# Performance work log

Measured on AMD Instinct MI355X. Metric: run time of the kernel, lower is better.

## Reference

```python
import jax, jax.numpy as jnp
import numpy as np

D_MODEL = 768


def setup_inputs() -> dict:
    key = jax.random.key(0)
    ks = jax.random.split(key, 16)
    B, S, D = 8, 2048, D_MODEL
    scale = 1.0 / np.sqrt(D)
    inp = {
        "Z_graph": jax.random.normal(ks[0], (B, S, D), dtype=jnp.float32),
        "Z_lstm": jax.random.normal(ks[1], (B, S, D), dtype=jnp.float32),
    }
    names = ["Wqg", "Wkl", "Wvl", "Wql", "Wkg", "Wvg", "Wf"]
    for i, n in enumerate(names):
        inp[n] = jax.random.uniform(ks[2 + i], (D, D), dtype=jnp.float32,
                                    minval=-scale, maxval=scale)
        inp["b" + n[1:]] = jax.random.uniform(ks[9 + i], (D,), dtype=jnp.float32,
                                              minval=-scale, maxval=scale)
    return inp


def reference(Z_graph, Z_lstm, Wqg, bqg, Wkl, bkl, Wvl, bvl,
              Wql, bql, Wkg, bkg, Wvg, bvg, Wf, bf):
    D = Z_graph.shape[-1]
    inv_sqrt_d = 1.0 / jnp.sqrt(jnp.asarray(D, dtype=Z_graph.dtype))

    def lin(x, W, b):
        # torch nn.Linear: x @ W.T + b
        return jnp.einsum("bsd,ed->bse", x, W) + b

    # graph -> lstm attention
    Qg = lin(Z_graph, Wqg, bqg)
    Kl = lin(Z_lstm, Wkl, bkl)
    Vl = lin(Z_lstm, Wvl, bvl)
    attn_g2l = jax.nn.softmax(
        jnp.einsum("bqd,bkd->bqk", Qg, Kl) * inv_sqrt_d, axis=-1)
    Z_g2l = jnp.einsum("bqk,bkd->bqd", attn_g2l, Vl)

    # lstm -> graph attention
    Ql = lin(Z_lstm, Wql, bql)
    Kg = lin(Z_graph, Wkg, bkg)
    Vg = lin(Z_graph, Wvg, bvg)
    attn_l2g = jax.nn.softmax(
        jnp.einsum("bqd,bkd->bqk", Ql, Kg) * inv_sqrt_d, axis=-1)
    Z_l2g = jnp.einsum("bqk,bkd->bqd", attn_l2g, Vg)

    Z_fused = Z_g2l + Z_l2g
    return lin(Z_fused, Wf, bf)
```

## Files before the change

kernel.cpp:

```cpp
#include <hip/hip_runtime.h>
#include <math.h>

#define TILE 128
#define BK   64
#define NT   256

typedef __attribute__((ext_vector_type(8))) short bf16x8;
typedef __attribute__((ext_vector_type(4))) float f32x4;

typedef const __attribute__((address_space(1))) void* gvp;
typedef __attribute__((address_space(3))) void* lvp;

__device__ __forceinline__ float bf2f(unsigned short u) {
  union { unsigned int i; float f; } v; v.i = ((unsigned int)u) << 16; return v.f;
}
__device__ __forceinline__ unsigned short f2bf(float f) {
  union { float ff; unsigned int i; } v; v.ff = f;
  return (unsigned short)((v.i + 0x7fffu + ((v.i >> 16) & 1u)) >> 16);
}

__device__ __forceinline__ int xcd_swz(int h, int nwg) {
  int q = nwg >> 3, r = nwg & 7;
  int xcd = h & 7, pos = h >> 3;
  return (xcd < r ? xcd * (q + 1) : r * (q + 1) + (xcd - r) * q) + pos;
}

struct GemmSrc { const unsigned short* A; int lda; const unsigned short* B; int ldb; int nk; };

__device__ __forceinline__ void stage_tile(const unsigned short* g, int ld, int r0, int k0,
                                           short* lds, int tid) {
#pragma unroll
  for (int i = 0; i < 4; ++i) {
    int cid = i * NT + tid;
    int row = cid >> 3, kc = cid & 7;
    int kcs = kc ^ (row & 7);
    const unsigned short* src = g + (size_t)(r0 + row) * ld + (k0 + kcs * 8);
    __builtin_amdgcn_global_load_lds((gvp)src, (lvp)(lds + cid * 8), 16, 0, 0);
  }
}

__device__ __forceinline__ void compute_tile(const short* As, const short* Bs,
                                             f32x4 acc[4][4], int lr, int lk, int wm, int wn) {
#pragma unroll
  for (int kk = 0; kk < 2; ++kk) {
    bf16x8 a[4], b[4];
#pragma unroll
    for (int i = 0; i < 4; ++i) {
      int ra = wm * 64 + i * 16 + lr;
      int rb = wn * 64 + i * 16 + lr;
      int ca = ((kk * 4 + lk) ^ (ra & 7)) * 8;
      int cb = ((kk * 4 + lk) ^ (rb & 7)) * 8;
      a[i] = *(const bf16x8*)(As + ra * BK + ca);
      b[i] = *(const bf16x8*)(Bs + rb * BK + cb);
    }
#pragma unroll
    for (int i = 0; i < 4; ++i)
#pragma unroll
      for (int j = 0; j < 4; ++j)
        acc[i][j] = __builtin_amdgcn_mfma_f32_16x16x32_bf16(a[i], b[j], acc[i][j], 0, 0, 0);
  }
}

template<int NS>
__device__ __forceinline__ void gemm_accum(const GemmSrc* s, f32x4 acc[4][4],
                                           short* As, short* Bs, int tid, int r0, int c0) {
  int lane = tid & 63, w = tid >> 6;
  int lr = lane & 15, lk = lane >> 4;
  int wm = w >> 1, wn = w & 1;
#pragma unroll
  for (int si = 0; si < NS; ++si) {
    int nk = s[si].nk;
    for (int kt = 0; kt < nk; ++kt) {
      __syncthreads();
      stage_tile(s[si].A, s[si].lda, r0, kt * BK, As, tid);
      stage_tile(s[si].B, s[si].ldb, c0, kt * BK, Bs, tid);
      __syncthreads();
      compute_tile(As, Bs, acc, lr, lk, wm, wn);
    }
  }
}

__device__ __forceinline__ void gemm_accum_pair(const unsigned short* A, int lda,
                                                const unsigned short* B, int ldb, int nk,
                                                f32x4 acc[4][4],
                                                short* A0, short* B0, short* A1, short* B1,
                                                int tid, int r0, int c0) {
  int lane = tid & 63, w = tid >> 6;
  int lr = lane & 15, lk = lane >> 4;
  int wm = w >> 1, wn = w & 1;
  for (int kt = 0; kt < nk / 2; ++kt) {
    __syncthreads();
    stage_tile(A, lda, r0, (2 * kt) * BK,     A0, tid);
    stage_tile(B, ldb, c0, (2 * kt) * BK,     B0, tid);
    stage_tile(A, lda, r0, (2 * kt + 1) * BK, A1, tid);
    stage_tile(B, ldb, c0, (2 * kt + 1) * BK, B1, tid);
    __syncthreads();
    compute_tile(A0, B0, acc, lr, lk, wm, wn);
    compute_tile(A1, B1, acc, lr, lk, wm, wn);
  }
}

template<bool OUT_BF16, bool BIAS_N, bool BIAS_M>
__device__ __forceinline__ void gemm_epilogue(f32x4 acc[4][4], void* C, int ldc,
                                              int r0, int c0, const float* bias,
                                              float alpha, int tid) {
  int lane = tid & 63, w = tid >> 6;
  int lr = lane & 15, lk = lane >> 4;
  int wm = w >> 1, wn = w & 1;
#pragma unroll
  for (int i = 0; i < 4; ++i) {
#pragma unroll
    for (int j = 0; j < 4; ++j) {
      int col = c0 + wn * 64 + j * 16 + lr;
      float bn = BIAS_N ? bias[col] : 0.f;
#pragma unroll
      for (int r = 0; r < 4; ++r) {
        int row = r0 + wm * 64 + i * 16 + lk * 4 + r;
        float v = acc[i][j][r] * alpha + bn;
        if (BIAS_M) v += bias[row];
        size_t idx = (size_t)row * ldc + col;
        if (OUT_BF16) ((unsigned short*)C)[idx] = f2bf(v);
        else          ((float*)C)[idx] = v;
      }
    }
  }
}

__device__ __forceinline__ void zero_acc(f32x4 acc[4][4]) {
  f32x4 z = { 0.f, 0.f, 0.f, 0.f };
#pragma unroll
  for (int i = 0; i < 4; ++i)
#pragma unroll
    for (int j = 0; j < 4; ++j) acc[i][j] = z;
}


struct ConvW { const float* src[7]; unsigned short* dst[7]; };

__global__ __launch_bounds__(NT) void k_convert_w(ConvW a) {
  int z = blockIdx.y;
  const float* s = a.src[z];
  unsigned short* d = a.dst[z];
  const int n = 768 * 768;
  int stride = gridDim.x * NT * 4;
  for (int i = ((int)blockIdx.x * NT + (int)threadIdx.x) * 4; i < n; i += stride) {
    float4 f = *(const float4*)(s + i);
    ushort4 o;
    o.x = f2bf(f.x); o.y = f2bf(f.y); o.z = f2bf(f.z); o.w = f2bf(f.w);
    *(ushort4*)(d + i) = o;
  }
}

__global__ __launch_bounds__(NT) void k_convert_z(const float* zg, const float* zl,
                                                  unsigned short* dg, unsigned short* dl,
                                                  float* lsum, int nL,
                                                  long long off, int n) {
  if (blockIdx.y == 0) {
    int fid = ((int)blockIdx.x * NT + (int)threadIdx.x) * 4;
    if (fid < nL) *(float4*)(lsum + fid) = make_float4(0.f, 0.f, 0.f, 0.f);
  }
  const float* s = (blockIdx.y ? zl : zg) + off;
  unsigned short* d = blockIdx.y ? dl : dg;
  int stride = gridDim.x * NT * 4;
  for (int i = ((int)blockIdx.x * NT + (int)threadIdx.x) * 4; i < n; i += stride) {
    float4 f = *(const float4*)(s + i);
    ushort4 o;
    o.x = f2bf(f.x); o.y = f2bf(f.y); o.z = f2bf(f.z); o.w = f2bf(f.w);
    *(ushort4*)(d + i) = o;
  }
}

struct ProjAllArgs {
  const unsigned short* A[6];
  const unsigned short* B[6];
  const float* bias[6];
  unsigned short* dst[6];
  int SG;
};

__global__ __launch_bounds__(512) void k_projall(ProjAllArgs p) {
  __shared__ __align__(16) short lds[4][TILE * BK];
  int nwg = (int)gridDim.x;
  int l = xcd_swz((int)blockIdx.x, nwg);
  int tpz = nwg / 6;
  int z = l / tpz, t = l % tpz;
  int grp = (int)threadIdx.x >> 8;
  int gt  = (int)threadIdx.x & 255;
  bool vt = (z >= 4);
  int r0, c0;
  if (!vt) { r0 = (t / 3) * TILE; c0 = ((t % 3) * 2 + grp) * TILE; }
  else     { r0 = ((t % 3) * 2 + grp) * TILE; c0 = (t / 3) * TILE; }
  f32x4 acc[4][4]; zero_acc(acc);
  GemmSrc s = { p.A[z], 768, p.B[z], 768, 768 / BK };
  gemm_accum<1>(&s, acc, lds[grp * 2], lds[grp * 2 + 1], gt, r0, c0);
  if (!vt)
    gemm_epilogue<true, true, false>(acc, p.dst[z], 768, r0, c0, p.bias[z], 1.f, gt);
  else
    gemm_epilogue<true, false, true>(acc, p.dst[z], p.SG, r0, c0, p.bias[z], 1.f, gt);
}

__global__ __launch_bounds__(512) void k_scores(const unsigned short* Qg, const unsigned short* Kl,
                                                const unsigned short* Ql, const unsigned short* Kg,
                                                unsigned short* S, float* lsum,
                                                float alpha, int G) {
  __shared__ __align__(16) short lds[4][TILE * BK];
  int nwg = (int)(gridDim.x * gridDim.y * gridDim.z);
  int h = (int)blockIdx.x + (int)gridDim.x * ((int)blockIdx.y + (int)gridDim.y * (int)blockIdx.z);
  int l = xcd_swz(h, nwg);
  int xp = l & 7, y = (l >> 3) & 15, z = l >> 7;
  int grp = (int)threadIdx.x >> 8;
  int gt  = (int)threadIdx.x & 255;
  int x = xp * 2 + grp;
  int dir = (z >= G) ? 1 : 0, gi = z - dir * G;
  const unsigned short* Q = (dir ? Ql : Qg) + (size_t)gi * 2048 * 768;
  const unsigned short* K = (dir ? Kg : Kl) + (size_t)gi * 2048 * 768;
  unsigned short* C = S + (size_t)z * 2048 * 2048;
  float* lrow = lsum + (size_t)z * 2048;
  int r0 = y * TILE, c0 = x * TILE;
  int lane = gt & 63, w = gt >> 6;
  int lr = lane & 15, lk = lane >> 4, wm = w >> 1, wn = w & 1;
  f32x4 acc[4][4]; zero_acc(acc);
  GemmSrc s = { Q, 768, K, 768, 768 / BK };
  gemm_accum<1>(&s, acc, lds[grp * 2], lds[grp * 2 + 1], gt, r0, c0);
  __syncthreads();
  short* Es = lds[grp * 2];
#pragma unroll
  for (int i = 0; i < 4; ++i) {
    float rs[4] = { 0.f, 0.f, 0.f, 0.f };
#pragma unroll
    for (int j = 0; j < 4; ++j) {
      int lcol = wn * 64 + j * 16 + lr;
#pragma unroll
      for (int r = 0; r < 4; ++r) {
        int lrw = wm * 64 + i * 16 + lk * 4 + r;
        unsigned short eb = f2bf(__expf(acc[i][j][r] * alpha));
        Es[lrw * TILE + (lcol ^ ((lrw & 7) << 4))] = (short)eb;
        rs[r] += bf2f(eb);
      }
    }
#pragma unroll
    for (int r = 0; r < 4; ++r) {
      float v = rs[r];
      v += __shfl_xor(v, 1); v += __shfl_xor(v, 2);
      v += __shfl_xor(v, 4); v += __shfl_xor(v, 8);
      if (lr == 0) atomicAdd(&lrow[r0 + wm * 64 + i * 16 + lk * 4 + r], v);
    }
  }
  __syncthreads();
#pragma unroll
  for (int c = 0; c < 8; ++c) {
    int id = c * 256 + gt;
    int lrw = id >> 4, cc = id & 15;
    uint4 v = *(const uint4*)(Es + lrw * TILE + ((cc * 8) ^ ((lrw & 7) << 4)));
    *(uint4*)(C + (size_t)(r0 + lrw) * 2048 + c0 + cc * 8) = v;
  }
}

__global__ __launch_bounds__(512) void k_pv(const unsigned short* S, const unsigned short* VlT,
                                            const unsigned short* VgT, const float* lsum,
                                            unsigned short* Zf, int G, int SG) {
  __shared__ __align__(16) short lds[4][TILE * BK];
  int nwg = (int)(gridDim.x * gridDim.y * gridDim.z);
  int h = (int)blockIdx.x + (int)gridDim.x * ((int)blockIdx.y + (int)gridDim.y * (int)blockIdx.z);
  int l = xcd_swz(h, nwg);
  int x = l % 6, t2 = l / 6;
  int y = t2 & 15, z = t2 >> 4;
  int r0 = y * TILE, c0 = x * TILE;
  int grp = (int)threadIdx.x >> 8;
  int gt  = (int)threadIdx.x & 255;
  f32x4 acc[4][4]; zero_acc(acc);
  GemmSrc s;
  if (grp == 0) s = { S + (size_t)z * 2048 * 2048,       2048, VlT + (size_t)z * 2048, SG, 2048 / BK };
  else          s = { S + (size_t)(G + z) * 2048 * 2048, 2048, VgT + (size_t)z * 2048, SG, 2048 / BK };
  gemm_accum<1>(&s, acc, lds[grp * 2], lds[grp * 2 + 1], gt, r0, c0);
  int lane = gt & 63, w = gt >> 6;
  int lr = lane & 15, lk = lane >> 4, wm = w >> 1, wn = w & 1;
  const float* lb = lsum + (size_t)(grp ? (G + z) : z) * 2048;
  float linv[4][4];
#pragma unroll
  for (int i = 0; i < 4; ++i)
#pragma unroll
    for (int r = 0; r < 4; ++r)
      linv[i][r] = 1.0f / lb[r0 + wm * 64 + i * 16 + lk * 4 + r];
#pragma unroll
  for (int i = 0; i < 4; ++i)
#pragma unroll
    for (int j = 0; j < 4; ++j)
#pragma unroll
      for (int r = 0; r < 4; ++r)
        acc[i][j][r] *= linv[i][r];
  float* red = (float*)lds;
  __syncthreads();
  if (grp == 1) {
#pragma unroll
    for (int i = 0; i < 4; ++i)
#pragma unroll
      for (int j = 0; j < 4; ++j)
#pragma unroll
        for (int r = 0; r < 4; ++r) {
          int row = wm * 64 + i * 16 + lk * 4 + r;
          int col = wn * 64 + j * 16 + lr;
          red[row * 128 + col] = acc[i][j][r];
        }
  }
  __syncthreads();
  if (grp == 0) {
#pragma unroll
    for (int i = 0; i < 4; ++i)
#pragma unroll
      for (int j = 0; j < 4; ++j)
#pragma unroll
        for (int r = 0; r < 4; ++r) {
          int row = wm * 64 + i * 16 + lk * 4 + r;
          int col = wn * 64 + j * 16 + lr;
          acc[i][j][r] += red[row * 128 + col];
        }
    gemm_epilogue<true, false, false>(acc, Zf + (size_t)z * 2048 * 768, 768, r0, c0,
                                      nullptr, 1.f, gt);
  }
}

__global__ __launch_bounds__(NT) void k_final(const unsigned short* Zf, const unsigned short* Wf,
                                              const float* bias, float* out) {
  __shared__ __align__(16) short sbuf[4 * TILE * BK];
  int nwg = (int)gridDim.x;
  int l = xcd_swz((int)blockIdx.x, nwg);
  int r0 = (l / 6) * TILE, c0 = (l % 6) * TILE;
  f32x4 acc[4][4]; zero_acc(acc);
  gemm_accum_pair(Zf, 768, Wf, 768, 768 / BK, acc,
                  sbuf, sbuf + TILE * BK, sbuf + 2 * TILE * BK, sbuf + 3 * TILE * BK,
                  threadIdx.x, r0, c0);
  gemm_epilogue<false, true, false>(acc, out, 768, r0, c0, bias, 1.f, threadIdx.x);
}


extern "C" void kernel_launch(void* const* d_in, const int* in_sizes, int n_in,
                              void* d_out, int out_size, void* d_ws, size_t ws_size,
                              hipStream_t stream) {
  const int B = 8, S = 2048, D = 768;

  const float* Zg  = (const float*)d_in[0];
  const float* Zl  = (const float*)d_in[1];
  const float* bqg = (const float*)d_in[3];
  const float* bkl = (const float*)d_in[5];
  const float* bvl = (const float*)d_in[7];
  const float* bql = (const float*)d_in[9];
  const float* bkg = (const float*)d_in[11];
  const float* bvg = (const float*)d_in[13];
  const float* bf  = (const float*)d_in[15];

  auto needG = [&](int G) -> size_t {
    size_t zrow = (size_t)G * S * D * 2;
    size_t sb = (size_t)2 * G * S * S * 2;
    size_t zbf = 2 * zrow;
    return 7 * ((size_t)D * D * 2) + 6 * zrow + (size_t)2 * G * S * 4
         + (sb > zbf ? sb : zbf) + (1u << 20);
  };
  int G = 1;
  if      (ws_size >= needG(8)) G = 8;
  else if (ws_size >= needG(4)) G = 4;
  else if (ws_size >= needG(2)) G = 2;
  const int SG = G * S;

  char* w = (char*)d_ws;
  size_t off = 0;
  auto alloc = [&](size_t bytes) -> char* {
    char* p = w + off; off += (bytes + 255) & ~(size_t)255; return p;
  };
  const size_t ZROW = (size_t)SG * D * 2;
  unsigned short* Wbf[7];
  for (int i = 0; i < 7; ++i) Wbf[i] = (unsigned short*)alloc((size_t)D * D * 2);
  unsigned short* QgZf  = (unsigned short*)alloc(ZROW);
  unsigned short* Kl    = (unsigned short*)alloc(ZROW);
  unsigned short* Ql    = (unsigned short*)alloc(ZROW);
  unsigned short* Kg    = (unsigned short*)alloc(ZROW);
  unsigned short* VlT   = (unsigned short*)alloc(ZROW);
  unsigned short* VgT   = (unsigned short*)alloc(ZROW);
  float* lsum = (float*)alloc((size_t)2 * G * S * 4);
  size_t ov = off;
  unsigned short* Zg_bf = (unsigned short*)alloc(ZROW);
  unsigned short* Zl_bf = (unsigned short*)alloc(ZROW);
  unsigned short* Sb    = (unsigned short*)(w + ov);

  ConvW cw;
  cw.src[0] = (const float*)d_in[2];  cw.src[1] = (const float*)d_in[4];
  cw.src[2] = (const float*)d_in[6];  cw.src[3] = (const float*)d_in[8];
  cw.src[4] = (const float*)d_in[10]; cw.src[5] = (const float*)d_in[12];
  cw.src[6] = (const float*)d_in[14];
  for (int i = 0; i < 7; ++i) cw.dst[i] = Wbf[i];
  k_convert_w<<<dim3(576, 7), NT, 0, stream>>>(cw);

  ProjAllArgs pj;
  pj.A[0] = Zg_bf;  pj.B[0] = Wbf[0]; pj.bias[0] = bqg; pj.dst[0] = QgZf;
  pj.A[1] = Zl_bf;  pj.B[1] = Wbf[1]; pj.bias[1] = bkl; pj.dst[1] = Kl;
  pj.A[2] = Zl_bf;  pj.B[2] = Wbf[3]; pj.bias[2] = bql; pj.dst[2] = Ql;
  pj.A[3] = Zg_bf;  pj.B[3] = Wbf[4]; pj.bias[3] = bkg; pj.dst[3] = Kg;
  pj.A[4] = Wbf[2]; pj.B[4] = Zl_bf;  pj.bias[4] = bvl; pj.dst[4] = VlT;
  pj.A[5] = Wbf[5]; pj.B[5] = Zg_bf;  pj.bias[5] = bvg; pj.dst[5] = VgT;
  pj.SG = SG;

  float alpha = 1.0f / sqrtf(768.0f);
  const int nZ = SG * D;
  const int nL = 2 * G * S;

  for (int b0 = 0; b0 < B; b0 += G) {
    k_convert_z<<<dim3(1024, 2), NT, 0, stream>>>(Zg, Zl, Zg_bf, Zl_bf, lsum, nL,
                                                  (long long)b0 * S * D, nZ);
    k_projall<<<dim3(6 * (SG / TILE) * 3), 512, 0, stream>>>(pj);
    k_scores<<<dim3(8, 16, 2 * G), 512, 0, stream>>>(QgZf, Kl, Ql, Kg, Sb, lsum, alpha, G);
    k_pv<<<dim3(6, 16, G), 512, 0, stream>>>(Sb, VlT, VgT, lsum, QgZf, G, SG);
    k_final<<<dim3(6 * (SG / TILE)), NT, 0, stream>>>(QgZf, Wbf[6], bf,
                                                      (float*)d_out + (size_t)b0 * S * D);
  }
}
```

Before: 447.4 us.

## Share activation tile across two projections per workgroup in projection kernel

The projection kernel now pairs two projections that read the same activation rows (Qg with Kg, Kl with Ql) in one 512-thread workgroup. The shared A tile is staged once into LDS by all 512 threads, and each 256-thread half stages its own weight tile. For the V-transposed projections, the shared Z tile is loaded once and reused across two weight row tiles. This cuts redundant global-to-LDS loads of the shared operand, at the cost of replacing the previous gemm_accum pipeline with a simple single-buffered loop that has two barriers per k-step.

Measured after the change: 443.1 us. No clear change (-1.0%).

```diff
diff --git a/kernel.cpp b/kernel.cpp
--- a/kernel.cpp
+++ b/kernel.cpp
@@ -32,6 +32,18 @@
 #pragma unroll
   for (int i = 0; i < 4; ++i) {
     int cid = i * NT + tid;
+    int row = cid >> 3, kc = cid & 7;
+    int kcs = kc ^ (row & 7);
+    const unsigned short* src = g + (size_t)(r0 + row) * ld + (k0 + kcs * 8);
+    __builtin_amdgcn_global_load_lds((gvp)src, (lvp)(lds + cid * 8), 16, 0, 0);
+  }
+}
+
+__device__ __forceinline__ void stage_tile512(const unsigned short* g, int ld, int r0, int k0,
+                                              short* lds, int tid) {
+#pragma unroll
+  for (int i = 0; i < 2; ++i) {
+    int cid = i * 512 + tid;
     int row = cid >> 3, kc = cid & 7;
     int kcs = kc ^ (row & 7);
     const unsigned short* src = g + (size_t)(r0 + row) * ld + (k0 + kcs * 8);
@@ -181,22 +193,43 @@
 __global__ __launch_bounds__(512) void k_projall(ProjAllArgs p) {
   __shared__ __align__(16) short lds[4][TILE * BK];
   int nwg = (int)gridDim.x;
+  int RT = p.SG / TILE;
   int l = xcd_swz((int)blockIdx.x, nwg);
-  int tpz = nwg / 6;
-  int z = l / tpz, t = l % tpz;
-  int grp = (int)threadIdx.x >> 8;
-  int gt  = (int)threadIdx.x & 255;
-  bool vt = (z >= 4);
-  int r0, c0;
-  if (!vt) { r0 = (t / 3) * TILE; c0 = ((t % 3) * 2 + grp) * TILE; }
-  else     { r0 = ((t % 3) * 2 + grp) * TILE; c0 = (t / 3) * TILE; }
+  int tid = (int)threadIdx.x;
+  int grp = tid >> 8, gt = tid & 255;
+  int lane = gt & 63, w = gt >> 6;
+  int lr = lane & 15, lk = lane >> 4, wm = w >> 1, wn = w & 1;
   f32x4 acc[4][4]; zero_acc(acc);
-  GemmSrc s = { p.A[z], 768, p.B[z], 768, 768 / BK };
-  gemm_accum<1>(&s, acc, lds[grp * 2], lds[grp * 2 + 1], gt, r0, c0);
-  if (!vt)
+  int nvt = 12 * RT;
+  if (l < nvt) {
+    int zp = l / (6 * RT), t = l % (6 * RT);
+    int r0 = (t / 6) * TILE, c0 = (t % 6) * TILE;
+    int z = zp == 0 ? (grp ? 3 : 0) : (grp ? 2 : 1);
+    const unsigned short* Asrc = p.A[z];
+    const unsigned short* Bsrc = p.B[z];
+    for (int kt = 0; kt < 768 / BK; ++kt) {
+      __syncthreads();
+      stage_tile512(Asrc, 768, r0, kt * BK, lds[0], tid);
+      stage_tile(Bsrc, 768, c0, kt * BK, lds[2 + grp], gt);
+      __syncthreads();
+      compute_tile(lds[0], lds[2 + grp], acc, lr, lk, wm, wn);
+    }
     gemm_epilogue<true, true, false>(acc, p.dst[z], 768, r0, c0, p.bias[z], 1.f, gt);
-  else
+  } else {
+    int lv = l - nvt;
+    int z = 4 + lv / (3 * RT), t = lv % (3 * RT);
+    int r0 = ((t % 3) * 2 + grp) * TILE, c0 = (t / 3) * TILE;
+    const unsigned short* Asrc = p.A[z];
+    const unsigned short* Bsrc = p.B[z];
+    for (int kt = 0; kt < 768 / BK; ++kt) {
+      __syncthreads();
+      stage_tile512(Bsrc, 768, c0, kt * BK, lds[0], tid);
+      stage_tile(Asrc, 768, r0, kt * BK, lds[2 + grp], gt);
+      __syncthreads();
+      compute_tile(lds[2 + grp], lds[0], acc, lr, lk, wm, wn);
+    }
     gemm_epilogue<true, false, true>(acc, p.dst[z], p.SG, r0, c0, p.bias[z], 1.f, gt);
+  }
 }
 
 __global__ __launch_bounds__(512) void k_scores(const unsigned short* Qg, const unsigned short* Kl,
@@ -402,11 +435,12 @@
   float alpha = 1.0f / sqrtf(768.0f);
   const int nZ = SG * D;
   const int nL = 2 * G * S;
+  const int RT = SG / TILE;
 
   for (int b0 = 0; b0 < B; b0 += G) {
     k_convert_z<<<dim3(1024, 2), NT, 0, stream>>>(Zg, Zl, Zg_bf, Zl_bf, lsum, nL,
                                                   (long long)b0 * S * D, nZ);
-    k_projall<<<dim3(6 * (SG / TILE) * 3), 512, 0, stream>>>(pj);
+    k_projall<<<dim3(18 * RT), 512, 0, stream>>>(pj);
     k_scores<<<dim3(8, 16, 2 * G), 512, 0, stream>>>(QgZf, Kl, Ql, Kg, Sb, lsum, alpha, G);
     k_pv<<<dim3(6, 16, G), 512, 0, stream>>>(Sb, VlT, VgT, lsum, QgZf, G, SG);
     k_final<<<dim3(6 * (SG / TILE)), NT, 0, stream>>>(QgZf, Wbf[6], bf,
```
